# Optimization experiments

Measured on AMD Instinct MI355X. Metric: run time of the kernel, lower is better.

Reference implementation:

```python
import jax, jax.numpy as jnp
import numpy as np

N = 100000      # nodes
E = 1600000     # edges (avg degree 16)
F_IN = 256
F_OUT = 128


def setup_inputs() -> dict:
    key = jax.random.key(0)
    k1, k2, k3, k4, k5 = jax.random.split(key, 5)
    x = jax.random.normal(k1, (N, F_IN), dtype=jnp.float32)
    adj_row = jax.random.randint(k2, (E,), 0, N, dtype=jnp.int32)
    adj_col = jax.random.randint(k3, (E,), 0, N, dtype=jnp.int32)
    adj_vals = jax.random.uniform(k4, (E,), dtype=jnp.float32)
    # he_uniform init for weight, zeros for bias (as in build())
    limit = jnp.sqrt(6.0 / F_IN)
    w = jax.random.uniform(k5, (F_IN, F_OUT), minval=-limit, maxval=limit, dtype=jnp.float32)
    b = jnp.zeros((F_OUT,), dtype=jnp.float32)
    return {"x": x, "adj_row": adj_row, "adj_col": adj_col, "adj_vals": adj_vals, "w": w, "b": b}


def reference(x, adj_row, adj_col, adj_vals, w, b):
    # dense feature transform: [N, F_in] @ [F_in, F_out] -> [N, F_out]
    h = x @ w
    # sparse adjacency SpMM (COO): out[r] += vals[e] * h[c] for edge e=(r,c)
    msgs = adj_vals[:, None] * h[adj_col]            # [E, F_out]
    agg = jax.ops.segment_sum(msgs, adj_row, num_segments=N)  # [N, F_out]
    # bias + relu activation
    return jax.nn.relu(agg + b)
```

## Files before the change

### kernel.cpp

```cpp
#include <hip/hip_runtime.h>
#include <hip/hip_bf16.h>
#include <cstdint>
#include <cstddef>

#define N_NODES 100000
#define N_EDGES 1600000
#define F_IN 256
#define F_OUT 128

#define NB 782
#define NBLK 196
#define TILE 8192
#define CAP 4096

typedef __attribute__((ext_vector_type(8))) short short8;
typedef __attribute__((ext_vector_type(4))) float floatx4;

static __device__ __forceinline__ unsigned short f2bf(float f) {
    union { float f; unsigned u; } v; v.f = f;
    unsigned r = v.u + 0x7FFF + ((v.u >> 16) & 1);
    return (unsigned short)(r >> 16);
}

__global__ void prep_w(const float* __restrict__ w, unsigned short* __restrict__ wT) {
    int i = blockIdx.x * 256 + threadIdx.x;
    int k = i >> 7;
    int n = i & 127;
    int g = (k >> 3) ^ (n & 7);
    wT[n * 256 + g * 8 + (k & 7)] = f2bf(w[i]);
}

__global__ __launch_bounds__(256, 2) void gemm_xw(const float* __restrict__ x,
                                                  const unsigned short* __restrict__ wT,
                                                  unsigned short* __restrict__ h) {
    __shared__ __align__(16) unsigned short wlds[128 * 256];
    const int tid = threadIdx.x;
    {
        const floatx4* src = reinterpret_cast<const floatx4*>(wT);
        floatx4* dst = reinterpret_cast<floatx4*>(wlds);
        #pragma unroll
        for (int i = 0; i < 16; i++) dst[tid + i * 256] = src[tid + i * 256];
    }
    __syncthreads();

    const int wave = tid >> 6, lane = tid & 63;
    const int quad = lane >> 4, l16 = lane & 15;
    const int rowbase = blockIdx.x * 256 + wave * 64;

    floatx4 acc[4][8];
    #pragma unroll
    for (int mf = 0; mf < 4; mf++)
        #pragma unroll
        for (int nt = 0; nt < 8; nt++) acc[mf][nt] = (floatx4)0.f;

    #pragma unroll
    for (int ks = 0; ks < 8; ks++) {
        const int k0 = ks * 32 + quad * 8;
        short8 afrag[4];
        #pragma unroll
        for (int mf = 0; mf < 4; mf++) {
            int row = rowbase + mf * 16 + l16;
            if (row >= N_NODES) row = N_NODES - 1;
            const float* xp = x + (size_t)row * F_IN + k0;
            floatx4 x0 = *reinterpret_cast<const floatx4*>(xp);
            floatx4 x1 = *reinterpret_cast<const floatx4*>(xp + 4);
            short8 a;
            a[0] = (short)f2bf(x0[0]); a[1] = (short)f2bf(x0[1]);
            a[2] = (short)f2bf(x0[2]); a[3] = (short)f2bf(x0[3]);
            a[4] = (short)f2bf(x1[0]); a[5] = (short)f2bf(x1[1]);
            a[6] = (short)f2bf(x1[2]); a[7] = (short)f2bf(x1[3]);
            afrag[mf] = a;
        }
        short8 bfrag[8];
        const int gq = ks * 4 + quad;
        #pragma unroll
        for (int nt = 0; nt < 8; nt++) {
            const int n = nt * 16 + l16;
            const int g = gq ^ (n & 7);
            bfrag[nt] = *reinterpret_cast<const short8*>(&wlds[n * 256 + g * 8]);
        }
        #pragma unroll
        for (int mf = 0; mf < 4; mf++)
            #pragma unroll
            for (int nt = 0; nt < 8; nt++)
                acc[mf][nt] = __builtin_amdgcn_mfma_f32_16x16x32_bf16(
                    afrag[mf], bfrag[nt], acc[mf][nt], 0, 0, 0);
    }

    #pragma unroll
    for (int mf = 0; mf < 4; mf++) {
        const int mbase = rowbase + mf * 16 + quad * 4;
        #pragma unroll
        for (int reg = 0; reg < 4; reg++) {
            const int m = mbase + reg;
            if (m < N_NODES) {
                #pragma unroll
                for (int nt = 0; nt < 8; nt++)
                    h[(size_t)m * F_OUT + nt * 16 + l16] = f2bf(acc[mf][nt][reg]);
            }
        }
    }
}

__global__ __launch_bounds__(256) void bucket_hist(const int* __restrict__ row,
                                                   int* __restrict__ bucket_total,
                                                   int* __restrict__ blockbase) {
    __shared__ int hist[NB];
    const int t = threadIdx.x, blk = blockIdx.x;
    for (int i = t; i < NB; i += 256) hist[i] = 0;
    __syncthreads();
    const long tb = (long)blk * TILE;
    #pragma unroll
    for (int c = 0; c < 8; c++) {
        long i0 = tb + c * 1024 + t * 4;
        if (i0 + 4 <= N_EDGES) {
            int4 r = *reinterpret_cast<const int4*>(row + i0);
            atomicAdd(&hist[r.x >> 7], 1); atomicAdd(&hist[r.y >> 7], 1);
            atomicAdd(&hist[r.z >> 7], 1); atomicAdd(&hist[r.w >> 7], 1);
        } else {
            for (long i = i0; i < N_EDGES && i < i0 + 4; i++)
                atomicAdd(&hist[row[i] >> 7], 1);
        }
    }
    __syncthreads();
    for (int bin = t; bin < NB; bin += 256)
        blockbase[bin * NBLK + blk] = atomicAdd(&bucket_total[bin], hist[bin]);
}

__global__ void bucket_scan(const int* __restrict__ bucket_total,
                            int* __restrict__ bucket_base) {
    __shared__ int sm[1024];
    const int t = threadIdx.x;
    int v = (t < NB) ? bucket_total[t] : 0;
    sm[t] = v; __syncthreads();
    for (int off = 1; off < 1024; off <<= 1) {
        int x2 = (t >= off) ? sm[t - off] : 0;
        __syncthreads();
        sm[t] += x2;
        __syncthreads();
    }
    if (t < NB) bucket_base[t] = sm[t] - v;
    if (t == NB - 1) bucket_base[NB] = sm[t];
}

__global__ __launch_bounds__(256) void bucket_scatter(const int* __restrict__ row,
                                                      const int* __restrict__ col,
                                                      const float* __restrict__ val,
                                                      const int* __restrict__ bucket_base,
                                                      const int* __restrict__ blockbase,
                                                      int2* __restrict__ metabuf) {
    __shared__ int sbase[NB];
    const int t = threadIdx.x, blk = blockIdx.x;
    for (int bin = t; bin < NB; bin += 256)
        sbase[bin] = bucket_base[bin] + blockbase[bin * NBLK + blk];
    __syncthreads();
    const long tb = (long)blk * TILE;
    #pragma unroll
    for (int c = 0; c < 8; c++) {
        long i0 = tb + c * 1024 + t * 4;
        if (i0 + 4 <= N_EDGES) {
            int4 r  = *reinterpret_cast<const int4*>(row + i0);
            int4 cc = *reinterpret_cast<const int4*>(col + i0);
            floatx4 vv = *reinterpret_cast<const floatx4*>(val + i0);
            int rr[4] = {r.x, r.y, r.z, r.w};
            int c4[4] = {cc.x, cc.y, cc.z, cc.w};
            float v4[4] = {vv[0], vv[1], vv[2], vv[3]};
            #pragma unroll
            for (int j = 0; j < 4; j++) {
                int bin = rr[j] >> 7, rl = rr[j] & 127;
                int pos = atomicAdd(&sbase[bin], 1);
                metabuf[pos] = make_int2(c4[j] | (rl << 24), __float_as_int(v4[j]));
            }
        } else {
            for (long i = i0; i < N_EDGES && i < i0 + 4; i++) {
                int rv = row[i];
                int bin = rv >> 7, rl = rv & 127;
                int pos = atomicAdd(&sbase[bin], 1);
                metabuf[pos] = make_int2(col[i] | (rl << 24), __float_as_int(val[i]));
            }
        }
    }
}

__global__ __launch_bounds__(256) void bucket_bin(const int* __restrict__ bucket_base,
                                                  int2* __restrict__ metabuf,
                                                  int* __restrict__ cnt,
                                                  int* __restrict__ row_start) {
    __shared__ int2 st[CAP];
    __shared__ int hist[128], scanb[128], cursor[128];
    const int t = threadIdx.x, b = blockIdx.x;
    const int b0 = bucket_base[b], e = bucket_base[b + 1];
    int n = e - b0; if (n > CAP) n = CAP;
    if (t < 128) hist[t] = 0;
    __syncthreads();
    for (int i = t; i < n; i += 256) {
        int2 w = metabuf[b0 + i];
        st[i] = w;
        atomicAdd(&hist[((unsigned)w.x >> 24) & 127], 1);
    }
    __syncthreads();
    if (t < 128) scanb[t] = hist[t];
    __syncthreads();
    for (int off = 1; off < 128; off <<= 1) {
        int v = (t >= off && t < 128) ? scanb[t - off] : 0;
        __syncthreads();
        if (t < 128) scanb[t] += v;
        __syncthreads();
    }
    if (t < 128) {
        int excl = scanb[t] - hist[t];
        cursor[t] = excl;
        int r = b * 128 + t;
        if (r < N_NODES) { cnt[r] = hist[t]; row_start[r] = b0 + excl; }
    }
    __syncthreads();
    for (int i = t; i < n; i += 256) {
        int2 w = st[i];
        int rl = ((unsigned)w.x >> 24) & 127;
        int pos = atomicAdd(&cursor[rl], 1);
        metabuf[b0 + pos] = make_int2(w.x & 0x00FFFFFF, w.y);
    }
}

__global__ __launch_bounds__(256) void spmm(const unsigned short* __restrict__ h,
                                            const int* __restrict__ row_start,
                                            const int* __restrict__ cnt,
                                            const int2* __restrict__ meta,
                                            const float* __restrict__ bias,
                                            float* __restrict__ out) {
    const int wave = threadIdx.x >> 6, lane = threadIdx.x & 63;
    const int g = lane >> 4, l16 = lane & 15;
    const int r = blockIdx.x * 4 + wave;
    if (r >= N_NODES) return;
    const int start = row_start[r], deg = cnt[r];

    float acc[8];
    #pragma unroll
    for (int d = 0; d < 8; d++) acc[d] = 0.f;

    const unsigned short* hp = h + l16 * 8;

    if (deg > 0) {
        for (int i = 0; i < deg; i += 16) {
            int2 mm[4];
            #pragma unroll
            for (int u = 0; u < 4; u++) {
                int idx = i + u * 4 + g;
                if (idx > deg - 1) idx = deg - 1;
                mm[u] = meta[start + idx];
            }
            uint4 hv[4];
            #pragma unroll
            for (int u = 0; u < 4; u++)
                hv[u] = *reinterpret_cast<const uint4*>(hp + (size_t)mm[u].x * F_OUT);
            #pragma unroll
            for (int u = 0; u < 4; u++) {
                float v = (i + u * 4 + g < deg) ? __int_as_float(mm[u].y) : 0.f;
                #pragma unroll
                for (int d = 0; d < 4; d++) {
                    unsigned uu = ((const unsigned*)&hv[u])[d];
                    acc[2 * d]     += v * __uint_as_float(uu << 16);
                    acc[2 * d + 1] += v * __uint_as_float(uu & 0xffff0000u);
                }
            }
        }
    }

    #pragma unroll
    for (int d = 0; d < 8; d++) {
        acc[d] += __shfl_xor(acc[d], 16);
        acc[d] += __shfl_xor(acc[d], 32);
    }
    float s0 = (g & 1) ? acc[2] : acc[0];
    float s1 = (g & 1) ? acc[3] : acc[1];
    float t0 = (g & 1) ? acc[6] : acc[4];
    float t1 = (g & 1) ? acc[7] : acc[5];
    float o0 = (g & 2) ? t0 : s0;
    float o1 = (g & 2) ? t1 : s1;
    const int ch = l16 * 8 + g * 2;
    o0 = fmaxf(o0 + bias[ch], 0.f);
    o1 = fmaxf(o1 + bias[ch + 1], 0.f);
    float2 o; o.x = o0; o.y = o1;
    *reinterpret_cast<float2*>(out + (size_t)r * F_OUT + ch) = o;
}

extern "C" void kernel_launch(void* const* d_in, const int* in_sizes, int n_in,
                              void* d_out, int out_size, void* d_ws, size_t ws_size,
                              hipStream_t stream) {
    const float* x        = (const float*)d_in[0];
    const int*   adj_row  = (const int*)d_in[1];
    const int*   adj_col  = (const int*)d_in[2];
    const float* adj_vals = (const float*)d_in[3];
    const float* w        = (const float*)d_in[4];
    const float* b        = (const float*)d_in[5];
    float* out = (float*)d_out;

    char* ws = (char*)d_ws;
    unsigned short* wT = (unsigned short*)ws;
    unsigned short* h  = (unsigned short*)(ws + 65536);
    size_t off = 65536 + (size_t)N_NODES * F_OUT * 2;
    int2* metabuf  = (int2*)(ws + off);   off += (size_t)N_EDGES * 8;
    int* cnt       = (int*)(ws + off);    off += (size_t)N_NODES * 4;
    int* row_start = (int*)(ws + off);    off += (size_t)N_NODES * 4;
    int* blockbase = (int*)(ws + off);    off += (size_t)NB * NBLK * 4;
    int* bucket_total = (int*)(ws + off); off += 3136;
    int* bucket_base  = (int*)(ws + off); off += 3136;

    prep_w<<<128, 256, 0, stream>>>(w, wT);
    hipMemsetAsync(bucket_total, 0, NB * 4, stream);
    gemm_xw<<<(N_NODES + 255) / 256, 256, 0, stream>>>(x, wT, h);
    bucket_hist<<<NBLK, 256, 0, stream>>>(adj_row, bucket_total, blockbase);
    bucket_scan<<<1, 1024, 0, stream>>>(bucket_total, bucket_base);
    bucket_scatter<<<NBLK, 256, 0, stream>>>(adj_row, adj_col, adj_vals,
                                             bucket_base, blockbase, metabuf);
    bucket_bin<<<NB, 256, 0, stream>>>(bucket_base, metabuf, cnt, row_start);
    spmm<<<N_NODES / 4, 256, 0, stream>>>(h, row_start, cnt, metabuf, b, out);
}
```

Baseline: 311.9 us.

## Fuse bucket row-binning into SpMM kernel using shared-memory edge lists

Merges the bucket_bin and spmm kernels. Each block takes one 128-row bucket, sorts its edges by local row into shared memory, then has 16-lane groups each compute four full rows directly. This removes the write-back of sorted metadata and the cnt/row_start arrays, drops one launch, and removes the cross-group shuffle reduction. In exchange only 782 blocks do all the gather work, which can leave the GPU underoccupied and load-imbalanced. Each 16-lane group walks its rows one edge at a time, which gives less memory-level parallelism per row.

```diff
diff --git a/kernel.cpp b/kernel.cpp
--- a/kernel.cpp
+++ b/kernel.cpp
@@ -182,22 +182,21 @@
     }
 }
 
-__global__ __launch_bounds__(256) void bucket_bin(const int* __restrict__ bucket_base,
-                                                  int2* __restrict__ metabuf,
-                                                  int* __restrict__ cnt,
-                                                  int* __restrict__ row_start) {
+__global__ __launch_bounds__(512, 8) void spmm_fused(const unsigned short* __restrict__ h,
+                                                     const int* __restrict__ bucket_base,
+                                                     const int2* __restrict__ meta,
+                                                     const float* __restrict__ bias,
+                                                     float* __restrict__ out) {
     __shared__ int2 st[CAP];
-    __shared__ int hist[128], scanb[128], cursor[128];
+    __shared__ int hist[128], scanb[128], startS[128], cursor[128];
     const int t = threadIdx.x, b = blockIdx.x;
-    const int b0 = bucket_base[b], e = bucket_base[b + 1];
-    int n = e - b0; if (n > CAP) n = CAP;
+    const int b0 = bucket_base[b];
+    int n = bucket_base[b + 1] - b0; if (n > CAP) n = CAP;
+
     if (t < 128) hist[t] = 0;
     __syncthreads();
-    for (int i = t; i < n; i += 256) {
-        int2 w = metabuf[b0 + i];
-        st[i] = w;
-        atomicAdd(&hist[((unsigned)w.x >> 24) & 127], 1);
-    }
+    for (int i = t; i < n; i += 512)
+        atomicAdd(&hist[((unsigned)meta[b0 + i].x >> 24) & 127], 1);
     __syncthreads();
     if (t < 128) scanb[t] = hist[t];
     __syncthreads();
@@ -207,47 +206,36 @@
         if (t < 128) scanb[t] += v;
         __syncthreads();
     }
-    if (t < 128) {
-        int excl = scanb[t] - hist[t];
-        cursor[t] = excl;
-        int r = b * 128 + t;
-        if (r < N_NODES) { cnt[r] = hist[t]; row_start[r] = b0 + excl; }
-    }
-    __syncthreads();
-    for (int i = t; i < n; i += 256) {
-        int2 w = st[i];
-        int rl = ((unsigned)w.x >> 24) & 127;
+    if (t < 128) { int e = scanb[t] - hist[t]; startS[t] = e; cursor[t] = e; }
+    __syncthreads();
+    for (int i = t; i < n; i += 512) {
+        int2 e = meta[b0 + i];
+        int rl = ((unsigned)e.x >> 24) & 127;
         int pos = atomicAdd(&cursor[rl], 1);
-        metabuf[b0 + pos] = make_int2(w.x & 0x00FFFFFF, w.y);
-    }
-}
-
-__global__ __launch_bounds__(256) void spmm(const unsigned short* __restrict__ h,
-                                            const int* __restrict__ row_start,
-                                            const int* __restrict__ cnt,
-                                            const int2* __restrict__ meta,
-                                            const float* __restrict__ bias,
-                                            float* __restrict__ out) {
-    const int wave = threadIdx.x >> 6, lane = threadIdx.x & 63;
-    const int g = lane >> 4, l16 = lane & 15;
-    const int r = blockIdx.x * 4 + wave;
-    if (r >= N_NODES) return;
-    const int start = row_start[r], deg = cnt[r];
-
-    float acc[8];
-    #pragma unroll
-    for (int d = 0; d < 8; d++) acc[d] = 0.f;
-
+        st[pos] = make_int2(e.x & 0x00FFFFFF, e.y);
+    }
+    __syncthreads();
+
+    const int lane = t & 63;
+    const int l16 = lane & 15;
+    const int grp = (t >> 6) * 4 + (lane >> 4);
     const unsigned short* hp = h + l16 * 8;
-
-    if (deg > 0) {
-        for (int i = 0; i < deg; i += 16) {
+    const floatx4 bv0 = *reinterpret_cast<const floatx4*>(bias + l16 * 8);
+    const floatx4 bv1 = *reinterpret_cast<const floatx4*>(bias + l16 * 8 + 4);
+
+    #pragma unroll
+    for (int j = 0; j < 4; j++) {
+        const int rl = grp * 4 + j;
+        const int s = startS[rl], d = hist[rl];
+        float acc[8];
+        #pragma unroll
+        for (int k = 0; k < 8; k++) acc[k] = 0.f;
+        for (int i = 0; i < d; i += 4) {
             int2 mm[4];
             #pragma unroll
             for (int u = 0; u < 4; u++) {
-                int idx = i + u * 4 + g;
-                if (idx > deg - 1) idx = deg - 1;
-                mm[u] = meta[start + idx];
+                int idx = i + u; if (idx > d - 1) idx = d - 1;
+                mm[u] = st[s + idx];
             }
             uint4 hv[4];
             #pragma unroll
@@ -255,33 +243,27 @@
                 hv[u] = *reinterpret_cast<const uint4*>(hp + (size_t)mm[u].x * F_OUT);
             #pragma unroll
             for (int u = 0; u < 4; u++) {
-                float v = (i + u * 4 + g < deg) ? __int_as_float(mm[u].y) : 0.f;
+                float v = (i + u < d) ? __int_as_float(mm[u].y) : 0.f;
                 #pragma unroll
-                for (int d = 0; d < 4; d++) {
-                    unsigned uu = ((const unsigned*)&hv[u])[d];
-                    acc[2 * d]     += v * __uint_as_float(uu << 16);
-                    acc[2 * d + 1] += v * __uint_as_float(uu & 0xffff0000u);
+                for (int k = 0; k < 4; k++) {
+                    unsigned uu = ((const unsigned*)&hv[u])[k];
+                    acc[2 * k]     += v * __uint_as_float(uu << 16);
+                    acc[2 * k + 1] += v * __uint_as_float(uu & 0xffff0000u);
                 }
             }
         }
-    }
-
-    #pragma unroll
-    for (int d = 0; d < 8; d++) {
-        acc[d] += __shfl_xor(acc[d], 16);
-        acc[d] += __shfl_xor(acc[d], 32);
-    }
-    float s0 = (g & 1) ? acc[2] : acc[0];
-    float s1 = (g & 1) ? acc[3] : acc[1];
-    float t0 = (g & 1) ? acc[6] : acc[4];
-    float t1 = (g & 1) ? acc[7] : acc[5];
-    float o0 = (g & 2) ? t0 : s0;
-    float o1 = (g & 2) ? t1 : s1;
-    const int ch = l16 * 8 + g * 2;
-    o0 = fmaxf(o0 + bias[ch], 0.f);
-    o1 = fmaxf(o1 + bias[ch + 1], 0.f);
-    float2 o; o.x = o0; o.y = o1;
-    *reinterpret_cast<float2*>(out + (size_t)r * F_OUT + ch) = o;
+        const int r = b * 128 + rl;
+        if (r < N_NODES) {
+            floatx4 o0, o1;
+            #pragma unroll
+            for (int k = 0; k < 4; k++) o0[k] = fmaxf(acc[k] + bv0[k], 0.f);
+            #pragma unroll
+            for (int k = 0; k < 4; k++) o1[k] = fmaxf(acc[4 + k] + bv1[k], 0.f);
+            float* op = out + (size_t)r * F_OUT + l16 * 8;
+            *reinterpret_cast<floatx4*>(op) = o0;
+            *reinterpret_cast<floatx4*>(op + 4) = o1;
+        }
+    }
 }
 
 extern "C" void kernel_launch(void* const* d_in, const int* in_sizes, int n_in,
@@ -300,8 +282,6 @@
     unsigned short* h  = (unsigned short*)(ws + 65536);
     size_t off = 65536 + (size_t)N_NODES * F_OUT * 2;
     int2* metabuf  = (int2*)(ws + off);   off += (size_t)N_EDGES * 8;
-    int* cnt       = (int*)(ws + off);    off += (size_t)N_NODES * 4;
-    int* row_start = (int*)(ws + off);    off += (size_t)N_NODES * 4;
     int* blockbase = (int*)(ws + off);    off += (size_t)NB * NBLK * 4;
     int* bucket_total = (int*)(ws + off); off += 3136;
     int* bucket_base  = (int*)(ws + off); off += 3136;
@@ -313,6 +293,5 @@
     bucket_scan<<<1, 1024, 0, stream>>>(bucket_total, bucket_base);
     bucket_scatter<<<NBLK, 256, 0, stream>>>(adj_row, adj_col, adj_vals,
                                              bucket_base, blockbase, metabuf);
-    bucket_bin<<<NB, 256, 0, stream>>>(bucket_base, metabuf, cnt, row_start);
-    spmm<<<N_NODES / 4, 256, 0, stream>>>(h, row_start, cnt, metabuf, b, out);
-}
+    spmm_fused<<<NB, 512, 0, stream>>>(h, bucket_base, metabuf, b, out);
+}
```

Measured after the change: 305.8 us. Within noise of the previous version (-2.0%).
